# Optimization experiments

Measured on AMD Instinct MI355X. Metric: run time of the kernel, lower is better.

## Reference

```python
import jax, jax.numpy as jnp
import numpy as np

HEADS = 4
DIM_HEAD = 64
INNER = HEADS * DIM_HEAD  # 256
MAP_SIZE = (8, 8, 8)
DN = ('NCDHW', 'OIDHW', 'NCDHW')


def _depthwise3d(x, w):
    # x: [B,C,D,H,W], w: [C,1,3,3,3] (torch groups=C layout)
    return jax.lax.conv_general_dilated(
        x, w, window_strides=(1, 1, 1), padding='SAME',
        dimension_numbers=DN, feature_group_count=x.shape[1])


def _dws_conv(x, dw, pw):
    # depthwise 3x3x3 then pointwise 1x1x1 (pw: [out,in])
    y = _depthwise3d(x, dw)
    return jnp.einsum('bcdhw,oc->bodhw', y, pw)


def _split_heads(t):
    # 'b (dim_head heads) d h w -> b heads (d h w) dim_head'
    B, C, D, H, W = t.shape
    t = t.reshape(B, DIM_HEAD, HEADS, D * H * W)
    return t.transpose(0, 2, 3, 1)


def _merge_heads(t, D, H, W):
    # 'b heads n dim_head -> b (dim_head heads) d h w'
    B = t.shape[0]
    return t.transpose(0, 3, 1, 2).reshape(B, DIM_HEAD * HEADS, D, H, W)


def setup_inputs() -> dict:
    key = jax.random.key(0)
    ks = jax.random.split(key, 8)
    B, feat_dim, map_dim, out_dim = 2, 128, 64, 128
    D = H = W = 24
    s = 0.02
    return {
        'feat': jax.random.normal(ks[0], (B, feat_dim, D, H, W), jnp.float32),
        'smap': jax.random.normal(ks[1], (B, map_dim) + MAP_SIZE, jnp.float32),
        'feat_qv_dw': jax.random.normal(ks[2], (feat_dim, 1, 3, 3, 3), jnp.float32) * s,
        'feat_qv_pw': jax.random.normal(ks[3], (2 * INNER, feat_dim), jnp.float32) * s,
        'feat_out_dw': jax.random.normal(ks[4], (INNER, 1, 3, 3, 3), jnp.float32) * s,
        'feat_out_pw': jax.random.normal(ks[5], (out_dim, INNER), jnp.float32) * s,
        'map_qv_w': jax.random.normal(ks[6], (2 * INNER, map_dim), jnp.float32) * s,
        'map_out_w': jax.random.normal(ks[7], (map_dim, INNER), jnp.float32) * s,
    }


def reference(feat, smap, feat_qv_dw, feat_qv_pw, feat_out_dw, feat_out_pw,
              map_qv_w, map_out_w):
    B, C, D, H, W = feat.shape
    scale = DIM_HEAD ** -0.5

    # projections
    fqv = _dws_conv(feat, feat_qv_dw, feat_qv_pw)           # [B, 2*inner, D,H,W]
    feat_q, feat_v = jnp.split(fqv, 2, axis=1)
    mqv = jnp.einsum('bcdhw,oc->bodhw', smap, map_qv_w)     # [B, 2*inner, 8,8,8]
    map_q, map_v = jnp.split(mqv, 2, axis=1)

    feat_q, feat_v = _split_heads(feat_q), _split_heads(feat_v)  # [B,h,N,dh]
    map_q, map_v = _split_heads(map_q), _split_heads(map_v)      # [B,h,M,dh]

    # shared scores, dual-direction softmax
    attn = jnp.einsum('bhid,bhjd->bhij', feat_q, map_q) * scale  # [B,h,N,M]
    feat_map_attn = jax.nn.softmax(attn, axis=-1)
    map_feat_attn = jax.nn.softmax(attn, axis=-2)

    feat_out = jnp.einsum('bhij,bhjd->bhid', feat_map_attn, map_v)   # [B,h,N,dh]
    map_out = jnp.einsum('bhji,bhjd->bhid', map_feat_attn, feat_v)   # [B,h,M,dh]

    feat_out = _merge_heads(feat_out, D, H, W)
    map_out = _merge_heads(map_out, *MAP_SIZE)

    feat_out = _dws_conv(feat_out, feat_out_dw, feat_out_pw)   # [B,out_dim,D,H,W]
    map_out = jnp.einsum('bcdhw,oc->bodhw', map_out, map_out_w)  # [B,map_dim,8,8,8]
    return feat_out, map_out
```

## Files before the change

### kernel.cpp

```cpp
#include <hip/hip_runtime.h>

#define BB 2
#define CH_FEAT 128
#define HEADS 4
#define DH 64
#define INNER 256
#define NPOS 13824
#define MPOS 512
#define DSZ 24
#define JSPLIT 27
#define JCHUNK (NPOS / JSPLIT)

typedef __attribute__((ext_vector_type(8))) short bf16x8;
typedef __attribute__((ext_vector_type(4))) float f32x4;

__device__ inline unsigned short bf16_rn(float x) {
  unsigned u = __builtin_bit_cast(unsigned, x);
  u += 0x7FFF + ((u >> 16) & 1);
  return (unsigned short)(u >> 16);
}
__device__ inline unsigned pk_bf16(float a, float b) {
  return (unsigned)bf16_rn(a) | ((unsigned)bf16_rn(b) << 16);
}
__device__ inline float bf2f(unsigned short u) {
  return __builtin_bit_cast(float, (unsigned)u << 16);
}
__device__ inline float4 ld_bf4(const unsigned short* p) {
  uint2 u = *(const uint2*)p;
  float4 f;
  f.x = __builtin_bit_cast(float, (u.x & 0xFFFFu) << 16);
  f.y = __builtin_bit_cast(float, u.x & 0xFFFF0000u);
  f.z = __builtin_bit_cast(float, (u.y & 0xFFFFu) << 16);
  f.w = __builtin_bit_cast(float, u.y & 0xFFFF0000u);
  return f;
}

#define GL2LDS(g, l)                                                        \
  __builtin_amdgcn_global_load_lds(                                         \
      (const __attribute__((address_space(1))) void*)(g),                   \
      (__attribute__((address_space(3))) void*)(l), 16, 0, 0)

__device__ inline bf16x8 lds_frag(const char* tile, int row, int colb) {
  return *(const bf16x8*)(tile + row * 128 + (colb ^ ((row & 7) << 4)));
}
__device__ inline bf16x8 lds_fragP(const char* tile, int row, int colb, int pitch) {
  return *(const bf16x8*)(tile + row * pitch + (colb ^ ((row & 7) << 4)));
}

__global__ __launch_bounds__(512) void k_map_qv(const float* __restrict__ smap,
                                                const float* __restrict__ w,
                                                unsigned short* __restrict__ mapqb,
                                                unsigned short* __restrict__ mapvTb) {
  int bm = blockIdx.x;
  int b = bm >> 9, m = bm & 511;
  __shared__ float s[64];
  int t = threadIdx.x;
  if (t < 64) s[t] = smap[(size_t)(b * 64 + t) * MPOS + m];
  __syncthreads();
  const float* wr = w + t * 64;
  float acc = 0.f;
#pragma unroll
  for (int c = 0; c < 64; ++c) acc += wr[c] * s[c];
  int qv = t >> 8, c2 = t & 255, head = c2 & 3, dh = c2 >> 2;
  int bh = b * HEADS + head;
  if (qv == 0)
    mapqb[((size_t)bh * MPOS + m) * 64 + dh] = bf16_rn(acc * 0.125f);
  else
    mapvTb[((size_t)bh * 64 + dh) * MPOS + m] = bf16_rn(acc);
}

__global__ __launch_bounds__(256) void k_dwf(const float* __restrict__ in,
                                             const float* __restrict__ w,
                                             unsigned short* __restrict__ out, int C) {
  int tid = blockIdx.x * 256 + threadIdx.x;
  int bc = tid / 1728;
  int s = tid - bc * 1728;
  int c = bc & (C - 1);
  int xs = (s % 3) * 8;
  int row = s / 3;
  int y = row % 24, z = row / 24;
  const float* wr = w + c * 27;
  const float* ip = in + (size_t)bc * NPOS;

  float acc[8];
#pragma unroll
  for (int i = 0; i < 8; ++i) acc[i] = 0.f;

#pragma unroll
  for (int dz = 0; dz < 3; ++dz) {
#pragma unroll
    for (int dy = 0; dy < 3; ++dy) {
      int zz = z + dz - 1, yy = y + dy - 1;
      bool ok = ((unsigned)zz < 24u) && ((unsigned)yy < 24u);
      float w0 = ok ? wr[dz * 9 + dy * 3 + 0] : 0.f;
      float w1 = ok ? wr[dz * 9 + dy * 3 + 1] : 0.f;
      float w2 = ok ? wr[dz * 9 + dy * 3 + 2] : 0.f;
      int zc = min(max(zz, 0), 23), yc = min(max(yy, 0), 23);
      int ro = (zc * 24 + yc) * 24;
      float4 Bv = *(const float4*)(ip + ro + xs);
      float4 Cv = *(const float4*)(ip + ro + xs + 4);
      float xm1 = xs ? *(ip + ro + xs - 1) : 0.f;
      float x8 = (xs < 16) ? *(ip + ro + xs + 8) : 0.f;
      float xv[10] = {xm1, Bv.x, Bv.y, Bv.z, Bv.w, Cv.x, Cv.y, Cv.z, Cv.w, x8};
#pragma unroll
      for (int i = 0; i < 8; ++i)
        acc[i] += w0 * xv[i] + w1 * xv[i + 1] + w2 * xv[i + 2];
    }
  }
  unsigned short* op = out + (size_t)bc * NPOS + row * 24 + xs;
  uint4 pv;
  pv.x = pk_bf16(acc[0], acc[1]);
  pv.y = pk_bf16(acc[2], acc[3]);
  pv.z = pk_bf16(acc[4], acc[5]);
  pv.w = pk_bf16(acc[6], acc[7]);
  *(uint4*)op = pv;
}

__global__ __launch_bounds__(256) void k_dwb(const unsigned short* __restrict__ in,
                                             const float* __restrict__ w,
                                             unsigned short* __restrict__ out, int C) {
  int tid = blockIdx.x * 256 + threadIdx.x;
  int bc = tid / 1728;
  int s = tid - bc * 1728;
  int c = bc & (C - 1), b = bc / C;
  int cm = (c & 63) * 4 + (c >> 6);
  int xs = (s % 3) * 8;
  int row = s / 3;
  int y = row % 24, z = row / 24;
  const float* wr = w + cm * 27;
  const unsigned short* ip = in + (size_t)bc * NPOS;

  float acc[8];
#pragma unroll
  for (int i = 0; i < 8; ++i) acc[i] = 0.f;

#pragma unroll
  for (int dz = 0; dz < 3; ++dz) {
#pragma unroll
    for (int dy = 0; dy < 3; ++dy) {
      int zz = z + dz - 1, yy = y + dy - 1;
      bool ok = ((unsigned)zz < 24u) && ((unsigned)yy < 24u);
      float w0 = ok ? wr[dz * 9 + dy * 3 + 0] : 0.f;
      float w1 = ok ? wr[dz * 9 + dy * 3 + 1] : 0.f;
      float w2 = ok ? wr[dz * 9 + dy * 3 + 2] : 0.f;
      int zc = min(max(zz, 0), 23), yc = min(max(yy, 0), 23);
      int ro = (zc * 24 + yc) * 24;
      float4 Bv = ld_bf4(ip + ro + xs);
      float4 Cv = ld_bf4(ip + ro + xs + 4);
      float xm1 = xs ? bf2f(ip[ro + xs - 1]) : 0.f;
      float x8 = (xs < 16) ? bf2f(ip[ro + xs + 8]) : 0.f;
      float xv[10] = {xm1, Bv.x, Bv.y, Bv.z, Bv.w, Cv.x, Cv.y, Cv.z, Cv.w, x8};
#pragma unroll
      for (int i = 0; i < 8; ++i)
        acc[i] += w0 * xv[i] + w1 * xv[i + 1] + w2 * xv[i + 2];
    }
  }
  unsigned short* op = out + ((size_t)b * C + cm) * NPOS + row * 24 + xs;
  uint4 pv;
  pv.x = pk_bf16(acc[0], acc[1]);
  pv.y = pk_bf16(acc[2], acc[3]);
  pv.z = pk_bf16(acc[4], acc[5]);
  pv.w = pk_bf16(acc[6], acc[7]);
  *(uint4*)op = pv;
}

__global__ __launch_bounds__(256) void k_pwqv_m(const unsigned short* __restrict__ dwt,
                                                const float* __restrict__ pw,
                                                unsigned short* __restrict__ fqb,
                                                unsigned short* __restrict__ fvTb) {
  __shared__ __align__(16) char sW[16384];
  __shared__ __align__(16) char sR[32768];
  __shared__ __align__(16) char sB[32768];
  int t = threadIdx.x, wave = t >> 6, lane = t & 63, g = lane >> 4, c = lane & 15;
  int n0 = blockIdx.x * 128, ti = blockIdx.y, b = blockIdx.z;
  int qv = ti >> 2, head = ti & 3, bh = b * 4 + head;

  {
    int r = t >> 2, ks = (t & 3) * 32;
    int co = qv * 256 + r * 4 + head;
    const float* wp = pw + (size_t)co * 128 + ks;
    unsigned pkv[16];
#pragma unroll
    for (int i = 0; i < 8; ++i) {
      float4 v = *(const float4*)(wp + i * 4);
      pkv[2 * i] = pk_bf16(v.x, v.y);
      pkv[2 * i + 1] = pk_bf16(v.z, v.w);
    }
#pragma unroll
    for (int u = 0; u < 4; ++u) {
      int colb = (ks * 2 + u * 16) ^ ((r & 7) << 4);
      *(uint4*)(sW + r * 256 + colb) = *(uint4*)&pkv[u * 4];
    }
  }
  const char* Bgc = (const char*)(dwt + (size_t)b * CH_FEAT * NPOS);
#pragma unroll
  for (int p = 0; p < 8; ++p) {
    int oo = p * 4096 + t * 16;
    int k = oo >> 8, col = oo & 255;
    GL2LDS(Bgc + (size_t)k * (NPOS * 2) + n0 * 2 + col, sR + oo);
  }
  __syncthreads();

  {
    const unsigned short* R16 = (const unsigned short*)sR;
#pragma unroll
    for (int it = 0; it < 8; ++it) {
      int cid = it * 256 + t;
      int n = cid & 127, kc16 = (cid >> 7) & 15;
      unsigned short v[8];
#pragma unroll
      for (int j = 0; j < 8; ++j) v[j] = R16[(kc16 * 8 + j) * 128 + n];
      unsigned u4[4];
#pragma unroll
      for (int i = 0; i < 4; ++i)
        u4[i] = (unsigned)v[2 * i] | ((unsigned)v[2 * i + 1] << 16);
      *(uint4*)(sB + n * 256 + ((kc16 * 16) ^ ((n & 7) << 4))) = *(uint4*)&u4[0];
    }
  }
  __syncthreads();

  f32x4 acc[4][2];
#pragma unroll
  for (int ct = 0; ct < 4; ++ct)
#pragma unroll
    for (int jf = 0; jf < 2; ++jf) acc[ct][jf] = (f32x4){0.f, 0.f, 0.f, 0.f};
  int nw = wave * 32;
#pragma unroll
  for (int kc = 0; kc < 4; ++kc) {
    bf16x8 bq[2];
#pragma unroll
    for (int jf = 0; jf < 2; ++jf)
      bq[jf] = lds_fragP(sB, nw + jf * 16 + c, kc * 64 + g * 16, 256);
#pragma unroll
    for (int ct = 0; ct < 4; ++ct) {
      bf16x8 a = lds_fragP(sW, ct * 16 + c, kc * 64 + g * 16, 256);
#pragma unroll
      for (int jf = 0; jf < 2; ++jf)
        acc[ct][jf] = __builtin_amdgcn_mfma_f32_16x16x32_bf16(a, bq[jf], acc[ct][jf], 0, 0, 0);
    }
  }
  __syncthreads();

  char* dmp = sR;
#pragma unroll
  for (int ct = 0; ct < 4; ++ct)
#pragma unroll
    for (int jf = 0; jf < 2; ++jf) {
      int n = nw + jf * 16 + c;
      uint2 wv;
      wv.x = pk_bf16(acc[ct][jf][0], acc[ct][jf][1]);
      wv.y = pk_bf16(acc[ct][jf][2], acc[ct][jf][3]);
      *(uint2*)(dmp + n * 144 + (ct * 16 + 4 * g) * 2) = wv;
    }
  __syncthreads();

  if (qv == 0) {
    int nr = t >> 1, seg = t & 1;
    const char* src = dmp + nr * 144 + seg * 64;
    unsigned short* dst = fqb + ((size_t)bh * NPOS + n0 + nr) * 64 + seg * 32;
#pragma unroll
    for (int i = 0; i < 4; ++i)
      *(uint4*)(dst + i * 8) = *(const uint4*)(src + i * 16);
  } else {
#pragma unroll
    for (int it = 0; it < 2; ++it) {
      int idx = it * 256 + t;
      int dh = idx >> 3, nseg = (idx & 7) * 16;
      unsigned pkv[8];
#pragma unroll
      for (int i = 0; i < 8; ++i) {
        unsigned short lo = *(const unsigned short*)(dmp + (nseg + 2 * i) * 144 + dh * 2);
        unsigned short hi = *(const unsigned short*)(dmp + (nseg + 2 * i + 1) * 144 + dh * 2);
        pkv[i] = (unsigned)lo | ((unsigned)hi << 16);
      }
      unsigned short* dst = fvTb + ((size_t)bh * 64 + dh) * NPOS + n0 + nseg;
      *(uint4*)(dst) = *(uint4*)&pkv[0];
      *(uint4*)(dst + 8) = *(uint4*)&pkv[4];
    }
  }
}

__global__ __launch_bounds__(256) void k_pwout_m(const unsigned short* __restrict__ dwo,
                                                 const float* __restrict__ pw,
                                                 float* __restrict__ out1) {
  __shared__ __align__(16) char sW[32768];
  __shared__ __align__(16) char sB[32768];
  __shared__ __align__(16) char sR[16384];
  int t = threadIdx.x, wave = t >> 6, lane = t & 63, g = lane >> 4, c = lane & 15;
  int n0 = blockIdx.x * 128, ti = blockIdx.y, b = blockIdx.z;

  {
    int r = t >> 2, ks = (t & 3) * 64;
    const float* wp = pw + (size_t)(ti * 64 + r) * 256 + ks;
    unsigned pkv[32];
#pragma unroll
    for (int i = 0; i < 16; ++i) {
      float4 v = *(const float4*)(wp + i * 4);
      pkv[2 * i] = pk_bf16(v.x, v.y);
      pkv[2 * i + 1] = pk_bf16(v.z, v.w);
    }
#pragma unroll
    for (int u = 0; u < 8; ++u) {
      int colb = (ks * 2 + u * 16) ^ ((r & 7) << 4);
      *(uint4*)(sW + r * 512 + colb) = *(uint4*)&pkv[u * 4];
    }
  }

  f32x4 acc[4][2];
#pragma unroll
  for (int ct = 0; ct < 4; ++ct)
#pragma unroll
    for (int jf = 0; jf < 2; ++jf) acc[ct][jf] = (f32x4){0.f, 0.f, 0.f, 0.f};
  int nw = wave * 32;
  const char* Bgc = (const char*)(dwo + (size_t)b * INNER * NPOS);
  const unsigned short* R16 = (const unsigned short*)sR;

  for (int kh = 0; kh < 2; ++kh) {
#pragma unroll
    for (int q = 0; q < 2; ++q) {
#pragma unroll
      for (int p = 0; p < 4; ++p) {
        int oo = p * 4096 + t * 16;
        int kl = oo >> 8, col = oo & 255;
        GL2LDS(Bgc + (size_t)(kh * 128 + q * 64 + kl) * (NPOS * 2) + n0 * 2 + col,
               sR + oo);
      }
      __syncthreads();
#pragma unroll
      for (int it = 0; it < 4; ++it) {
        int cid = it * 256 + t;
        int n = cid & 127, kcl = (cid >> 7) & 7;
        unsigned short v[8];
#pragma unroll
        for (int j = 0; j < 8; ++j) v[j] = R16[(kcl * 8 + j) * 128 + n];
        unsigned u4[4];
#pragma unroll
        for (int i = 0; i < 4; ++i)
          u4[i] = (unsigned)v[2 * i] | ((unsigned)v[2 * i + 1] << 16);
        int kc16 = q * 8 + kcl;
        *(uint4*)(sB + n * 256 + ((kc16 * 16) ^ ((n & 7) << 4))) = *(uint4*)&u4[0];
      }
      __syncthreads();
    }
#pragma unroll
    for (int kc = 0; kc < 4; ++kc) {
      bf16x8 bq[2];
#pragma unroll
      for (int jf = 0; jf < 2; ++jf)
        bq[jf] = lds_fragP(sB, nw + jf * 16 + c, kc * 64 + g * 16, 256);
#pragma unroll
      for (int ct = 0; ct < 4; ++ct) {
        bf16x8 a = lds_fragP(sW, ct * 16 + c, (kh * 4 + kc) * 64 + g * 16, 512);
#pragma unroll
        for (int jf = 0; jf < 2; ++jf)
          acc[ct][jf] = __builtin_amdgcn_mfma_f32_16x16x32_bf16(a, bq[jf], acc[ct][jf], 0, 0, 0);
      }
    }
    __syncthreads();
  }
#pragma unroll
  for (int ct = 0; ct < 4; ++ct)
#pragma unroll
    for (int jf = 0; jf < 2; ++jf) {
      int n = n0 + nw + jf * 16 + c;
#pragma unroll
      for (int r = 0; r < 4; ++r) {
        int co = ti * 64 + ct * 16 + 4 * g + r;
        out1[((size_t)b * 128 + co) * NPOS + n] = acc[ct][jf][r];
      }
    }
}

__global__ __launch_bounds__(256) void k_attn_row(const unsigned short* __restrict__ fqb,
                                                  const unsigned short* __restrict__ mapqb,
                                                  const unsigned short* __restrict__ mapvTb,
                                                  unsigned short* __restrict__ F) {
  __shared__ __align__(16) char sPool[32768];
  __shared__ __align__(16) unsigned sP[4][2][16][36];
  __shared__ float sL[4][2][16];
  int t = threadIdx.x, wave = t >> 6, lane = t & 63, g = lane >> 4, c = lane & 15;
  int bh = blockIdx.y;
  int j0 = blockIdx.x * 128 + wave * 32;

  const char* Kg = (const char*)(mapqb + (size_t)bh * MPOS * 64);
  const char* Vg = (const char*)(mapvTb + (size_t)bh * 64 * MPOS);

  const unsigned short* fqp = fqb + ((size_t)bh * NPOS + j0 + c) * 64 + 8 * g;
  bf16x8 bq00 = *(const bf16x8*)(fqp);
  bf16x8 bq01 = *(const bf16x8*)(fqp + 32);
  bf16x8 bq10 = *(const bf16x8*)(fqp + 16 * 64);
  bf16x8 bq11 = *(const bf16x8*)(fqp + 16 * 64 + 32);

  f32x4 o[2][4];
#pragma unroll
  for (int jf = 0; jf < 2; ++jf)
#pragma unroll
    for (int dt = 0; dt < 4; ++dt) o[jf][dt] = (f32x4){0.f, 0.f, 0.f, 0.f};
  float ls0 = 0.f, ls1 = 0.f;

#pragma unroll
  for (int p = 0; p < 2; ++p) {
    int oo = p * 4096 + t * 16;
    int row = oo >> 7, col = (oo & 127) ^ (((oo >> 7) & 7) << 4);
    GL2LDS(Kg + (size_t)row * 128 + col, sPool + oo);
    GL2LDS(Vg + (size_t)row * 1024 + col, sPool + 16384 + oo);
  }
  __syncthreads();

  for (int ic = 0; ic < 8; ++ic) {
    const char* Kt = sPool + (ic & 1) * 8192;
    const char* Vt = sPool + 16384 + (ic & 1) * 8192;
    if (ic < 7) {
      int ibase = (ic + 1) * 64;
      int bsel = ((ic + 1) & 1) * 8192;
#pragma unroll
      for (int p = 0; p < 2; ++p) {
        int oo = p * 4096 + t * 16;
        int row = oo >> 7, col = (oo & 127) ^ (((oo >> 7) & 7) << 4);
        GL2LDS(Kg + (size_t)(ibase + row) * 128 + col, sPool + bsel + oo);
        GL2LDS(Vg + (size_t)row * 1024 + ibase * 2 + col, sPool + 16384 + bsel + oo);
      }
    }
#pragma unroll
    for (int ti = 0; ti < 4; ++ti) {
      bf16x8 a0 = lds_frag(Kt, ti * 16 + c, 16 * g);
      bf16x8 a1 = lds_frag(Kt, ti * 16 + c, 64 + 16 * g);
      f32x4 s0 = {0.f, 0.f, 0.f, 0.f}, s1 = {0.f, 0.f, 0.f, 0.f};
      s0 = __builtin_amdgcn_mfma_f32_16x16x32_bf16(a0, bq00, s0, 0, 0, 0);
      s0 = __builtin_amdgcn_mfma_f32_16x16x32_bf16(a1, bq01, s0, 0, 0, 0);
      s1 = __builtin_amdgcn_mfma_f32_16x16x32_bf16(a0, bq10, s1, 0, 0, 0);
      s1 = __builtin_amdgcn_mfma_f32_16x16x32_bf16(a1, bq11, s1, 0, 0, 0);
      float p0 = __expf(s0[0]), p1 = __expf(s0[1]), p2 = __expf(s0[2]), p3 = __expf(s0[3]);
      ls0 += (p0 + p1) + (p2 + p3);
      sP[wave][0][c][ti * 8 + 2 * g] = pk_bf16(p0, p1);
      sP[wave][0][c][ti * 8 + 2 * g + 1] = pk_bf16(p2, p3);
      float q0 = __expf(s1[0]), q1 = __expf(s1[1]), q2 = __expf(s1[2]), q3 = __expf(s1[3]);
      ls1 += (q0 + q1) + (q2 + q3);
      sP[wave][1][c][ti * 8 + 2 * g] = pk_bf16(q0, q1);
      sP[wave][1][c][ti * 8 + 2 * g + 1] = pk_bf16(q2, q3);
    }
#pragma unroll
    for (int ks = 0; ks < 2; ++ks) {
      bf16x8 ap0 = *(const bf16x8*)&sP[wave][0][c][ks * 16 + 4 * g];
      bf16x8 ap1 = *(const bf16x8*)&sP[wave][1][c][ks * 16 + 4 * g];
#pragma unroll
      for (int dt = 0; dt < 4; ++dt) {
        bf16x8 bv = lds_frag(Vt, dt * 16 + c, ks * 64 + 16 * g);
        o[0][dt] = __builtin_amdgcn_mfma_f32_16x16x32_bf16(ap0, bv, o[0][dt], 0, 0, 0);
        o[1][dt] = __builtin_amdgcn_mfma_f32_16x16x32_bf16(ap1, bv, o[1][dt], 0, 0, 0);
      }
    }
    __syncthreads();
  }

  ls0 += __shfl_xor(ls0, 16); ls0 += __shfl_xor(ls0, 32);
  ls1 += __shfl_xor(ls1, 16); ls1 += __shfl_xor(ls1, 32);
  if (g == 0) { sL[wave][0][c] = 1.f / ls0; sL[wave][1][c] = 1.f / ls1; }
#pragma unroll
  for (int jf = 0; jf < 2; ++jf) {
    float rl0 = sL[wave][jf][4 * g + 0], rl1 = sL[wave][jf][4 * g + 1];
    float rl2 = sL[wave][jf][4 * g + 2], rl3 = sL[wave][jf][4 * g + 3];
#pragma unroll
    for (int dt = 0; dt < 4; ++dt) {
      uint2 wv;
      wv.x = pk_bf16(o[jf][dt][0] * rl0, o[jf][dt][1] * rl1);
      wv.y = pk_bf16(o[jf][dt][2] * rl2, o[jf][dt][3] * rl3);
      *(uint2*)(sPool + (dt * 16 + c) * 272 + (wave * 32 + jf * 16 + 4 * g) * 2) = wv;
    }
  }
  __syncthreads();
  {
    int ch = t >> 2, seg = t & 3;
    int b = bh >> 2, head = bh & 3;
    unsigned short* dst = F + ((size_t)b * INNER + head * 64 + ch) * NPOS +
                          blockIdx.x * 128 + seg * 32;
    const char* src = sPool + ch * 272 + seg * 64;
#pragma unroll
    for (int i = 0; i < 4; ++i)
      *(uint4*)(dst + i * 8) = *(const uint4*)(src + i * 16);
  }
}

__global__ __launch_bounds__(256) void k_attn_col(const unsigned short* __restrict__ fqb,
                                                  const unsigned short* __restrict__ fvTb,
                                                  const unsigned short* __restrict__ mapqb,
                                                  float* __restrict__ Gc,
                                                  float* __restrict__ Gl) {
  __shared__ __align__(16) char sQ[2][8192];
  __shared__ __align__(16) char sV[2][8192];
  __shared__ __align__(16) unsigned sP[4][2][16][36];
  int t = threadIdx.x, wave = t >> 6, lane = t & 63, g = lane >> 4, c = lane & 15;
  int bh = blockIdx.x, chunk = blockIdx.z;
  int i0 = blockIdx.y * 128 + wave * 32;
  int jb = chunk * JCHUNK;

  const char* Qg = (const char*)(fqb + (size_t)bh * NPOS * 64);
  const char* Vg = (const char*)(fvTb + (size_t)bh * 64 * NPOS);

  const unsigned short* kp = mapqb + ((size_t)bh * MPOS + i0 + c) * 64 + 8 * g;
  bf16x8 bm00 = *(const bf16x8*)(kp);
  bf16x8 bm01 = *(const bf16x8*)(kp + 32);
  bf16x8 bm10 = *(const bf16x8*)(kp + 16 * 64);
  bf16x8 bm11 = *(const bf16x8*)(kp + 16 * 64 + 32);

  f32x4 o[2][4];
#pragma unroll
  for (int f = 0; f < 2; ++f)
#pragma unroll
    for (int dt = 0; dt < 4; ++dt) o[f][dt] = (f32x4){0.f, 0.f, 0.f, 0.f};
  float lc0 = 0.f, lc1 = 0.f;

#pragma unroll
  for (int p = 0; p < 2; ++p) {
    int oo = p * 4096 + t * 16;
    int row = oo >> 7, col = (oo & 127) ^ (((oo >> 7) & 7) << 4);
    GL2LDS(Qg + (size_t)(jb + row) * 128 + col, sQ[0] + oo);
    GL2LDS(Vg + (size_t)row * (NPOS * 2) + jb * 2 + col, sV[0] + oo);
  }
  __syncthreads();

  for (int jc = 0; jc < JCHUNK / 64; ++jc) {
    const char* Qt = sQ[jc & 1];
    const char* Vt = sV[jc & 1];
    if (jc < JCHUNK / 64 - 1) {
      int jbase = jb + (jc + 1) * 64;
#pragma unroll
      for (int p = 0; p < 2; ++p) {
        int oo = p * 4096 + t * 16;
        int row = oo >> 7, col = (oo & 127) ^ (((oo >> 7) & 7) << 4);
        GL2LDS(Qg + (size_t)(jbase + row) * 128 + col, sQ[(jc + 1) & 1] + oo);
        GL2LDS(Vg + (size_t)row * (NPOS * 2) + jbase * 2 + col, sV[(jc + 1) & 1] + oo);
      }
    }
#pragma unroll
    for (int tj = 0; tj < 4; ++tj) {
      bf16x8 a0 = lds_frag(Qt, tj * 16 + c, 16 * g);
      bf16x8 a1 = lds_frag(Qt, tj * 16 + c, 64 + 16 * g);
      f32x4 s0 = {0.f, 0.f, 0.f, 0.f}, s1 = {0.f, 0.f, 0.f, 0.f};
      s0 = __builtin_amdgcn_mfma_f32_16x16x32_bf16(a0, bm00, s0, 0, 0, 0);
      s0 = __builtin_amdgcn_mfma_f32_16x16x32_bf16(a1, bm01, s0, 0, 0, 0);
      s1 = __builtin_amdgcn_mfma_f32_16x16x32_bf16(a0, bm10, s1, 0, 0, 0);
      s1 = __builtin_amdgcn_mfma_f32_16x16x32_bf16(a1, bm11, s1, 0, 0, 0);
      float p0 = __expf(s0[0]), p1 = __expf(s0[1]), p2 = __expf(s0[2]), p3 = __expf(s0[3]);
      lc0 += (p0 + p1) + (p2 + p3);
      sP[wave][0][c][tj * 8 + 2 * g] = pk_bf16(p0, p1);
      sP[wave][0][c][tj * 8 + 2 * g + 1] = pk_bf16(p2, p3);
      float q0 = __expf(s1[0]), q1 = __expf(s1[1]), q2 = __expf(s1[2]), q3 = __expf(s1[3]);
      lc1 += (q0 + q1) + (q2 + q3);
      sP[wave][1][c][tj * 8 + 2 * g] = pk_bf16(q0, q1);
      sP[wave][1][c][tj * 8 + 2 * g + 1] = pk_bf16(q2, q3);
    }
#pragma unroll
    for (int ks = 0; ks < 2; ++ks) {
      bf16x8 ap0 = *(const bf16x8*)&sP[wave][0][c][ks * 16 + 4 * g];
      bf16x8 ap1 = *(const bf16x8*)&sP[wave][1][c][ks * 16 + 4 * g];
#pragma unroll
      for (int dt = 0; dt < 4; ++dt) {
        bf16x8 bv = lds_frag(Vt, dt * 16 + c, ks * 64 + 16 * g);
        o[0][dt] = __builtin_amdgcn_mfma_f32_16x16x32_bf16(ap0, bv, o[0][dt], 0, 0, 0);
        o[1][dt] = __builtin_amdgcn_mfma_f32_16x16x32_bf16(ap1, bv, o[1][dt], 0, 0, 0);
      }
    }
    __syncthreads();
  }

  lc0 += __shfl_xor(lc0, 16); lc0 += __shfl_xor(lc0, 32);
  lc1 += __shfl_xor(lc1, 16); lc1 += __shfl_xor(lc1, 32);
  int gi = chunk * 8 + bh;
  if (g == 0) {
    Gl[(size_t)gi * MPOS + i0 + c] = lc0;
    Gl[(size_t)gi * MPOS + i0 + 16 + c] = lc1;
  }
  float* gp = Gc + ((size_t)gi * MPOS + i0) * 64;
#pragma unroll
  for (int f = 0; f < 2; ++f)
#pragma unroll
    for (int dt = 0; dt < 4; ++dt)
#pragma unroll
      for (int r = 0; r < 4; ++r)
        gp[(size_t)(f * 16 + 4 * g + r) * 64 + dt * 16 + c] = o[f][dt][r];
}

__global__ __launch_bounds__(256) void k_map_out(const float* __restrict__ Gc,
                                                 const float* __restrict__ Gl,
                                                 const float* __restrict__ mow,
                                                 float* __restrict__ out2) {
  int m = blockIdx.x, b = blockIdx.y, t = threadIdx.x;
  __shared__ float sMA[256];
  __shared__ float sL[4];
  if (t < 4) {
    float l = 0.f;
#pragma unroll 4
    for (int ch = 0; ch < JSPLIT; ++ch) l += Gl[(size_t)(ch * 8 + b * 4 + t) * MPOS + m];
    sL[t] = 1.f / l;
  }
  __syncthreads();
  {
    int head = t & 3, dh = t >> 2;
    int bh = b * 4 + head;
    float a = 0.f;
#pragma unroll 4
    for (int ch = 0; ch < JSPLIT; ++ch)
      a += Gc[((size_t)(ch * 8 + bh) * MPOS + m) * 64 + dh];
    sMA[t] = a * sL[head];
  }
  __syncthreads();
  if (t < 64) {
    const float* wr = mow + t * 256;
    float acc = 0.f;
#pragma unroll 4
    for (int c = 0; c < 256; ++c) acc += wr[c] * sMA[c];
    out2[((size_t)b * 64 + t) * MPOS + m] = acc;
  }
}

extern "C" void kernel_launch(void* const* d_in, const int* in_sizes, int n_in,
                              void* d_out, int out_size, void* d_ws, size_t ws_size,
                              hipStream_t stream) {
  const float* feat = (const float*)d_in[0];
  const float* smap = (const float*)d_in[1];
  const float* fqv_dw = (const float*)d_in[2];
  const float* fqv_pw = (const float*)d_in[3];
  const float* fout_dw = (const float*)d_in[4];
  const float* fout_pw = (const float*)d_in[5];
  const float* mqv_w = (const float*)d_in[6];
  const float* mout_w = (const float*)d_in[7];

  float* out = (float*)d_out;
  float* out1 = out;
  float* out2 = out + (size_t)BB * 128 * NPOS;

  const size_t QV = (size_t)BB * HEADS * NPOS * DH;
  const size_t MQV = (size_t)BB * HEADS * MPOS * DH;
  float* ws = (float*)d_ws;
  unsigned short* F = (unsigned short*)ws;
  unsigned short* fqb = (unsigned short*)(ws + QV);
  unsigned short* fvTb = fqb + QV;
  unsigned short* mapqb = fvTb + QV;
  unsigned short* mapvTb = mapqb + MQV;
  float* Gc = (float*)(mapvTb + MQV);
  float* Gl = Gc + (size_t)JSPLIT * 8 * MPOS * 64;

  unsigned short* dwt = (unsigned short*)out1;
  unsigned short* dwt2 = fqb;

  k_map_qv<<<dim3(BB * MPOS), dim3(512), 0, stream>>>(smap, mqv_w, mapqb, mapvTb);
  k_dwf<<<dim3(BB * CH_FEAT * 1728 / 256), dim3(256), 0, stream>>>(feat, fqv_dw, dwt, CH_FEAT);
  k_pwqv_m<<<dim3(NPOS / 128, 8, BB), dim3(256), 0, stream>>>(dwt, fqv_pw, fqb, fvTb);
  k_attn_row<<<dim3(NPOS / 128, BB * HEADS), dim3(256), 0, stream>>>(fqb, mapqb, mapvTb, F);
  k_attn_col<<<dim3(8, MPOS / 128, JSPLIT), dim3(256), 0, stream>>>(fqb, fvTb, mapqb, Gc, Gl);
  k_map_out<<<dim3(MPOS, BB), dim3(256), 0, stream>>>(Gc, Gl, mout_w, out2);
  k_dwb<<<dim3(BB * INNER * 1728 / 256), dim3(256), 0, stream>>>(F, fout_dw, dwt2, INNER);
  k_pwout_m<<<dim3(NPOS / 128, 2, BB), dim3(256), 0, stream>>>(dwt2, fout_pw, out1);
}
```

Before: 195.9 us.

## Merge independent kernels into combined launches via block-index dispatch

Three kernel pairs that don't depend on each other now each share one launch, with the block index choosing the branch: map QV projection with the first depthwise conv, row and column attention, and map output projection with the second depthwise conv. This cuts the launch count from eight to five, removes the gaps between back-to-back launches, and lets the small grids run alongside the large ones. The merged kernels take the larger shared-memory footprint and register pressure of either branch, which can lower occupancy for the lighter branch.

```diff
diff --git a/kernel.cpp b/kernel.cpp
--- a/kernel.cpp
+++ b/kernel.cpp
@@ -47,121 +47,77 @@
   return *(const bf16x8*)(tile + row * pitch + (colb ^ ((row & 7) << 4)));
 }
 
-__global__ __launch_bounds__(512) void k_map_qv(const float* __restrict__ smap,
-                                                const float* __restrict__ w,
-                                                unsigned short* __restrict__ mapqb,
-                                                unsigned short* __restrict__ mapvTb) {
-  int bm = blockIdx.x;
-  int b = bm >> 9, m = bm & 511;
-  __shared__ float s[64];
+__global__ __launch_bounds__(256) void k_pre(const float* __restrict__ smap,
+                                             const float* __restrict__ mqv_w,
+                                             unsigned short* __restrict__ mapqb,
+                                             unsigned short* __restrict__ mapvTb,
+                                             const float* __restrict__ feat,
+                                             const float* __restrict__ fqv_dw,
+                                             unsigned short* __restrict__ dwt) {
+  int bid = blockIdx.x;
   int t = threadIdx.x;
-  if (t < 64) s[t] = smap[(size_t)(b * 64 + t) * MPOS + m];
-  __syncthreads();
-  const float* wr = w + t * 64;
-  float acc = 0.f;
-#pragma unroll
-  for (int c = 0; c < 64; ++c) acc += wr[c] * s[c];
-  int qv = t >> 8, c2 = t & 255, head = c2 & 3, dh = c2 >> 2;
-  int bh = b * HEADS + head;
-  if (qv == 0)
-    mapqb[((size_t)bh * MPOS + m) * 64 + dh] = bf16_rn(acc * 0.125f);
-  else
-    mapvTb[((size_t)bh * 64 + dh) * MPOS + m] = bf16_rn(acc);
-}
-
-__global__ __launch_bounds__(256) void k_dwf(const float* __restrict__ in,
-                                             const float* __restrict__ w,
-                                             unsigned short* __restrict__ out, int C) {
-  int tid = blockIdx.x * 256 + threadIdx.x;
-  int bc = tid / 1728;
-  int s = tid - bc * 1728;
-  int c = bc & (C - 1);
-  int xs = (s % 3) * 8;
-  int row = s / 3;
-  int y = row % 24, z = row / 24;
-  const float* wr = w + c * 27;
-  const float* ip = in + (size_t)bc * NPOS;
-
-  float acc[8];
-#pragma unroll
-  for (int i = 0; i < 8; ++i) acc[i] = 0.f;
-
-#pragma unroll
-  for (int dz = 0; dz < 3; ++dz) {
-#pragma unroll
-    for (int dy = 0; dy < 3; ++dy) {
-      int zz = z + dz - 1, yy = y + dy - 1;
-      bool ok = ((unsigned)zz < 24u) && ((unsigned)yy < 24u);
-      float w0 = ok ? wr[dz * 9 + dy * 3 + 0] : 0.f;
-      float w1 = ok ? wr[dz * 9 + dy * 3 + 1] : 0.f;
-      float w2 = ok ? wr[dz * 9 + dy * 3 + 2] : 0.f;
-      int zc = min(max(zz, 0), 23), yc = min(max(yy, 0), 23);
-      int ro = (zc * 24 + yc) * 24;
-      float4 Bv = *(const float4*)(ip + ro + xs);
-      float4 Cv = *(const float4*)(ip + ro + xs + 4);
-      float xm1 = xs ? *(ip + ro + xs - 1) : 0.f;
-      float x8 = (xs < 16) ? *(ip + ro + xs + 8) : 0.f;
-      float xv[10] = {xm1, Bv.x, Bv.y, Bv.z, Bv.w, Cv.x, Cv.y, Cv.z, Cv.w, x8};
-#pragma unroll
-      for (int i = 0; i < 8; ++i)
-        acc[i] += w0 * xv[i] + w1 * xv[i + 1] + w2 * xv[i + 2];
-    }
-  }
-  unsigned short* op = out + (size_t)bc * NPOS + row * 24 + xs;
-  uint4 pv;
-  pv.x = pk_bf16(acc[0], acc[1]);
-  pv.y = pk_bf16(acc[2], acc[3]);
-  pv.z = pk_bf16(acc[4], acc[5]);
-  pv.w = pk_bf16(acc[6], acc[7]);
-  *(uint4*)op = pv;
-}
-
-__global__ __launch_bounds__(256) void k_dwb(const unsigned short* __restrict__ in,
-                                             const float* __restrict__ w,
-                                             unsigned short* __restrict__ out, int C) {
-  int tid = blockIdx.x * 256 + threadIdx.x;
-  int bc = tid / 1728;
-  int s = tid - bc * 1728;
-  int c = bc & (C - 1), b = bc / C;
-  int cm = (c & 63) * 4 + (c >> 6);
-  int xs = (s % 3) * 8;
-  int row = s / 3;
-  int y = row % 24, z = row / 24;
-  const float* wr = w + cm * 27;
-  const unsigned short* ip = in + (size_t)bc * NPOS;
-
-  float acc[8];
-#pragma unroll
-  for (int i = 0; i < 8; ++i) acc[i] = 0.f;
-
-#pragma unroll
-  for (int dz = 0; dz < 3; ++dz) {
-#pragma unroll
-    for (int dy = 0; dy < 3; ++dy) {
-      int zz = z + dz - 1, yy = y + dy - 1;
-      bool ok = ((unsigned)zz < 24u) && ((unsigned)yy < 24u);
-      float w0 = ok ? wr[dz * 9 + dy * 3 + 0] : 0.f;
-      float w1 = ok ? wr[dz * 9 + dy * 3 + 1] : 0.f;
-      float w2 = ok ? wr[dz * 9 + dy * 3 + 2] : 0.f;
-      int zc = min(max(zz, 0), 23), yc = min(max(yy, 0), 23);
-      int ro = (zc * 24 + yc) * 24;
-      float4 Bv = ld_bf4(ip + ro + xs);
-      float4 Cv = ld_bf4(ip + ro + xs + 4);
-      float xm1 = xs ? bf2f(ip[ro + xs - 1]) : 0.f;
-      float x8 = (xs < 16) ? bf2f(ip[ro + xs + 8]) : 0.f;
-      float xv[10] = {xm1, Bv.x, Bv.y, Bv.z, Bv.w, Cv.x, Cv.y, Cv.z, Cv.w, x8};
-#pragma unroll
-      for (int i = 0; i < 8; ++i)
-        acc[i] += w0 * xv[i] + w1 * xv[i + 1] + w2 * xv[i + 2];
-    }
-  }
-  unsigned short* op = out + ((size_t)b * C + cm) * NPOS + row * 24 + xs;
-  uint4 pv;
-  pv.x = pk_bf16(acc[0], acc[1]);
-  pv.y = pk_bf16(acc[2], acc[3]);
-  pv.z = pk_bf16(acc[4], acc[5]);
-  pv.w = pk_bf16(acc[6], acc[7]);
-  *(uint4*)op = pv;
+  if (bid < 1024) {
+    int b = bid >> 9, m = bid & 511;
+    __shared__ float s[64];
+    if (t < 64) s[t] = smap[(size_t)(b * 64 + t) * MPOS + m];
+    __syncthreads();
+#pragma unroll
+    for (int half = 0; half < 2; ++half) {
+      int co2 = half * 256 + t;
+      const float* wr = mqv_w + (size_t)co2 * 64;
+      float acc = 0.f;
+#pragma unroll
+      for (int c = 0; c < 64; ++c) acc += wr[c] * s[c];
+      int qv = co2 >> 8, c2 = co2 & 255, head = c2 & 3, dh = c2 >> 2;
+      int bh = b * HEADS + head;
+      if (qv == 0)
+        mapqb[((size_t)bh * MPOS + m) * 64 + dh] = bf16_rn(acc * 0.125f);
+      else
+        mapvTb[((size_t)bh * 64 + dh) * MPOS + m] = bf16_rn(acc);
+    }
+  } else {
+    int tid = (bid - 1024) * 256 + t;
+    int bc = tid / 1728;
+    int s = tid - bc * 1728;
+    int c = bc & (CH_FEAT - 1);
+    int xs = (s % 3) * 8;
+    int row = s / 3;
+    int y = row % 24, z = row / 24;
+    const float* wr = fqv_dw + c * 27;
+    const float* ip = feat + (size_t)bc * NPOS;
+
+    float acc[8];
+#pragma unroll
+    for (int i = 0; i < 8; ++i) acc[i] = 0.f;
+#pragma unroll
+    for (int dz = 0; dz < 3; ++dz) {
+#pragma unroll
+      for (int dy = 0; dy < 3; ++dy) {
+        int zz = z + dz - 1, yy = y + dy - 1;
+        bool ok = ((unsigned)zz < 24u) && ((unsigned)yy < 24u);
+        float w0 = ok ? wr[dz * 9 + dy * 3 + 0] : 0.f;
+        float w1 = ok ? wr[dz * 9 + dy * 3 + 1] : 0.f;
+        float w2 = ok ? wr[dz * 9 + dy * 3 + 2] : 0.f;
+        int zc = min(max(zz, 0), 23), yc = min(max(yy, 0), 23);
+        int ro = (zc * 24 + yc) * 24;
+        float4 Bv = *(const float4*)(ip + ro + xs);
+        float4 Cv = *(const float4*)(ip + ro + xs + 4);
+        float xm1 = xs ? *(ip + ro + xs - 1) : 0.f;
+        float x8 = (xs < 16) ? *(ip + ro + xs + 8) : 0.f;
+        float xv[10] = {xm1, Bv.x, Bv.y, Bv.z, Bv.w, Cv.x, Cv.y, Cv.z, Cv.w, x8};
+#pragma unroll
+        for (int i = 0; i < 8; ++i)
+          acc[i] += w0 * xv[i] + w1 * xv[i + 1] + w2 * xv[i + 2];
+      }
+    }
+    unsigned short* op = dwt + (size_t)bc * NPOS + row * 24 + xs;
+    uint4 pv;
+    pv.x = pk_bf16(acc[0], acc[1]);
+    pv.y = pk_bf16(acc[2], acc[3]);
+    pv.z = pk_bf16(acc[4], acc[5]);
+    pv.w = pk_bf16(acc[6], acc[7]);
+    *(uint4*)op = pv;
+  }
 }
 
 __global__ __launch_bounds__(256) void k_pwqv_m(const unsigned short* __restrict__ dwt,
@@ -280,6 +236,302 @@
   }
 }
 
+__global__ __launch_bounds__(256) void k_attn(const unsigned short* __restrict__ fqb,
+                                              const unsigned short* __restrict__ fvTb,
+                                              const unsigned short* __restrict__ mapqb,
+                                              const unsigned short* __restrict__ mapvTb,
+                                              unsigned short* __restrict__ F,
+                                              float* __restrict__ Gc,
+                                              float* __restrict__ Gl) {
+  __shared__ __align__(16) char sPool[32768];
+  __shared__ __align__(16) unsigned sP[4][2][16][36];
+  __shared__ __align__(16) float sL[4][2][16];
+  int bid = blockIdx.x;
+  int t = threadIdx.x, wave = t >> 6, lane = t & 63, g = lane >> 4, c = lane & 15;
+
+  if (bid < 864) {
+    int jblk = bid % 108, bh = bid / 108;
+    int j0 = jblk * 128 + wave * 32;
+
+    const char* Kg = (const char*)(mapqb + (size_t)bh * MPOS * 64);
+    const char* Vg = (const char*)(mapvTb + (size_t)bh * 64 * MPOS);
+
+    const unsigned short* fqp = fqb + ((size_t)bh * NPOS + j0 + c) * 64 + 8 * g;
+    bf16x8 bq00 = *(const bf16x8*)(fqp);
+    bf16x8 bq01 = *(const bf16x8*)(fqp + 32);
+    bf16x8 bq10 = *(const bf16x8*)(fqp + 16 * 64);
+    bf16x8 bq11 = *(const bf16x8*)(fqp + 16 * 64 + 32);
+
+    f32x4 o[2][4];
+#pragma unroll
+    for (int jf = 0; jf < 2; ++jf)
+#pragma unroll
+      for (int dt = 0; dt < 4; ++dt) o[jf][dt] = (f32x4){0.f, 0.f, 0.f, 0.f};
+    float ls0 = 0.f, ls1 = 0.f;
+
+#pragma unroll
+    for (int p = 0; p < 2; ++p) {
+      int oo = p * 4096 + t * 16;
+      int row = oo >> 7, col = (oo & 127) ^ (((oo >> 7) & 7) << 4);
+      GL2LDS(Kg + (size_t)row * 128 + col, sPool + oo);
+      GL2LDS(Vg + (size_t)row * 1024 + col, sPool + 16384 + oo);
+    }
+    __syncthreads();
+
+    for (int ic = 0; ic < 8; ++ic) {
+      const char* Kt = sPool + (ic & 1) * 8192;
+      const char* Vt = sPool + 16384 + (ic & 1) * 8192;
+      if (ic < 7) {
+        int ibase = (ic + 1) * 64;
+        int bsel = ((ic + 1) & 1) * 8192;
+#pragma unroll
+        for (int p = 0; p < 2; ++p) {
+          int oo = p * 4096 + t * 16;
+          int row = oo >> 7, col = (oo & 127) ^ (((oo >> 7) & 7) << 4);
+          GL2LDS(Kg + (size_t)(ibase + row) * 128 + col, sPool + bsel + oo);
+          GL2LDS(Vg + (size_t)row * 1024 + ibase * 2 + col, sPool + 16384 + bsel + oo);
+        }
+      }
+#pragma unroll
+      for (int ti = 0; ti < 4; ++ti) {
+        bf16x8 a0 = lds_frag(Kt, ti * 16 + c, 16 * g);
+        bf16x8 a1 = lds_frag(Kt, ti * 16 + c, 64 + 16 * g);
+        f32x4 s0 = {0.f, 0.f, 0.f, 0.f}, s1 = {0.f, 0.f, 0.f, 0.f};
+        s0 = __builtin_amdgcn_mfma_f32_16x16x32_bf16(a0, bq00, s0, 0, 0, 0);
+        s0 = __builtin_amdgcn_mfma_f32_16x16x32_bf16(a1, bq01, s0, 0, 0, 0);
+        s1 = __builtin_amdgcn_mfma_f32_16x16x32_bf16(a0, bq10, s1, 0, 0, 0);
+        s1 = __builtin_amdgcn_mfma_f32_16x16x32_bf16(a1, bq11, s1, 0, 0, 0);
+        float p0 = __expf(s0[0]), p1 = __expf(s0[1]), p2 = __expf(s0[2]), p3 = __expf(s0[3]);
+        ls0 += (p0 + p1) + (p2 + p3);
+        sP[wave][0][c][ti * 8 + 2 * g] = pk_bf16(p0, p1);
+        sP[wave][0][c][ti * 8 + 2 * g + 1] = pk_bf16(p2, p3);
+        float q0 = __expf(s1[0]), q1 = __expf(s1[1]), q2 = __expf(s1[2]), q3 = __expf(s1[3]);
+        ls1 += (q0 + q1) + (q2 + q3);
+        sP[wave][1][c][ti * 8 + 2 * g] = pk_bf16(q0, q1);
+        sP[wave][1][c][ti * 8 + 2 * g + 1] = pk_bf16(q2, q3);
+      }
+#pragma unroll
+      for (int ks = 0; ks < 2; ++ks) {
+        bf16x8 ap0 = *(const bf16x8*)&sP[wave][0][c][ks * 16 + 4 * g];
+        bf16x8 ap1 = *(const bf16x8*)&sP[wave][1][c][ks * 16 + 4 * g];
+#pragma unroll
+        for (int dt = 0; dt < 4; ++dt) {
+          bf16x8 bv = lds_frag(Vt, dt * 16 + c, ks * 64 + 16 * g);
+          o[0][dt] = __builtin_amdgcn_mfma_f32_16x16x32_bf16(ap0, bv, o[0][dt], 0, 0, 0);
+          o[1][dt] = __builtin_amdgcn_mfma_f32_16x16x32_bf16(ap1, bv, o[1][dt], 0, 0, 0);
+        }
+      }
+      __syncthreads();
+    }
+
+    ls0 += __shfl_xor(ls0, 16); ls0 += __shfl_xor(ls0, 32);
+    ls1 += __shfl_xor(ls1, 16); ls1 += __shfl_xor(ls1, 32);
+    if (g == 0) { sL[wave][0][c] = 1.f / ls0; sL[wave][1][c] = 1.f / ls1; }
+#pragma unroll
+    for (int jf = 0; jf < 2; ++jf) {
+      float rl0 = sL[wave][jf][4 * g + 0], rl1 = sL[wave][jf][4 * g + 1];
+      float rl2 = sL[wave][jf][4 * g + 2], rl3 = sL[wave][jf][4 * g + 3];
+#pragma unroll
+      for (int dt = 0; dt < 4; ++dt) {
+        uint2 wv;
+        wv.x = pk_bf16(o[jf][dt][0] * rl0, o[jf][dt][1] * rl1);
+        wv.y = pk_bf16(o[jf][dt][2] * rl2, o[jf][dt][3] * rl3);
+        *(uint2*)(sPool + (dt * 16 + c) * 272 + (wave * 32 + jf * 16 + 4 * g) * 2) = wv;
+      }
+    }
+    __syncthreads();
+    {
+      int ch = t >> 2, seg = t & 3;
+      int b = bh >> 2, head = bh & 3;
+      unsigned short* dst = F + ((size_t)b * INNER + head * 64 + ch) * NPOS +
+                            jblk * 128 + seg * 32;
+      const char* src = sPool + ch * 272 + seg * 64;
+#pragma unroll
+      for (int i = 0; i < 4; ++i)
+        *(uint4*)(dst + i * 8) = *(const uint4*)(src + i * 16);
+    }
+  } else {
+    int cid = bid - 864;
+    int bh = cid & 7, iblk = (cid >> 3) & 3, chunk = cid >> 5;
+    char* sQ = sPool;
+    char* sV = sPool + 16384;
+    int i0 = iblk * 128 + wave * 32;
+    int jb = chunk * JCHUNK;
+
+    const char* Qg = (const char*)(fqb + (size_t)bh * NPOS * 64);
+    const char* Vg = (const char*)(fvTb + (size_t)bh * 64 * NPOS);
+
+    const unsigned short* kp = mapqb + ((size_t)bh * MPOS + i0 + c) * 64 + 8 * g;
+    bf16x8 bm00 = *(const bf16x8*)(kp);
+    bf16x8 bm01 = *(const bf16x8*)(kp + 32);
+    bf16x8 bm10 = *(const bf16x8*)(kp + 16 * 64);
+    bf16x8 bm11 = *(const bf16x8*)(kp + 16 * 64 + 32);
+
+    f32x4 o[2][4];
+#pragma unroll
+    for (int f = 0; f < 2; ++f)
+#pragma unroll
+      for (int dt = 0; dt < 4; ++dt) o[f][dt] = (f32x4){0.f, 0.f, 0.f, 0.f};
+    float lc0 = 0.f, lc1 = 0.f;
+
+#pragma unroll
+    for (int p = 0; p < 2; ++p) {
+      int oo = p * 4096 + t * 16;
+      int row = oo >> 7, col = (oo & 127) ^ (((oo >> 7) & 7) << 4);
+      GL2LDS(Qg + (size_t)(jb + row) * 128 + col, sQ + oo);
+      GL2LDS(Vg + (size_t)row * (NPOS * 2) + jb * 2 + col, sV + oo);
+    }
+    __syncthreads();
+
+    for (int jc = 0; jc < JCHUNK / 64; ++jc) {
+      const char* Qt = sQ + (jc & 1) * 8192;
+      const char* Vt = sV + (jc & 1) * 8192;
+      if (jc < JCHUNK / 64 - 1) {
+        int jbase = jb + (jc + 1) * 64;
+        int bsel = ((jc + 1) & 1) * 8192;
+#pragma unroll
+        for (int p = 0; p < 2; ++p) {
+          int oo = p * 4096 + t * 16;
+          int row = oo >> 7, col = (oo & 127) ^ (((oo >> 7) & 7) << 4);
+          GL2LDS(Qg + (size_t)(jbase + row) * 128 + col, sQ + bsel + oo);
+          GL2LDS(Vg + (size_t)row * (NPOS * 2) + jbase * 2 + col, sV + bsel + oo);
+        }
+      }
+#pragma unroll
+      for (int tj = 0; tj < 4; ++tj) {
+        bf16x8 a0 = lds_frag(Qt, tj * 16 + c, 16 * g);
+        bf16x8 a1 = lds_frag(Qt, tj * 16 + c, 64 + 16 * g);
+        f32x4 s0 = {0.f, 0.f, 0.f, 0.f}, s1 = {0.f, 0.f, 0.f, 0.f};
+        s0 = __builtin_amdgcn_mfma_f32_16x16x32_bf16(a0, bm00, s0, 0, 0, 0);
+        s0 = __builtin_amdgcn_mfma_f32_16x16x32_bf16(a1, bm01, s0, 0, 0, 0);
+        s1 = __builtin_amdgcn_mfma_f32_16x16x32_bf16(a0, bm10, s1, 0, 0, 0);
+        s1 = __builtin_amdgcn_mfma_f32_16x16x32_bf16(a1, bm11, s1, 0, 0, 0);
+        float p0 = __expf(s0[0]), p1 = __expf(s0[1]), p2 = __expf(s0[2]), p3 = __expf(s0[3]);
+        lc0 += (p0 + p1) + (p2 + p3);
+        sP[wave][0][c][tj * 8 + 2 * g] = pk_bf16(p0, p1);
+        sP[wave][0][c][tj * 8 + 2 * g + 1] = pk_bf16(p2, p3);
+        float q0 = __expf(s1[0]), q1 = __expf(s1[1]), q2 = __expf(s1[2]), q3 = __expf(s1[3]);
+        lc1 += (q0 + q1) + (q2 + q3);
+        sP[wave][1][c][tj * 8 + 2 * g] = pk_bf16(q0, q1);
+        sP[wave][1][c][tj * 8 + 2 * g + 1] = pk_bf16(q2, q3);
+      }
+#pragma unroll
+      for (int ks = 0; ks < 2; ++ks) {
+        bf16x8 ap0 = *(const bf16x8*)&sP[wave][0][c][ks * 16 + 4 * g];
+        bf16x8 ap1 = *(const bf16x8*)&sP[wave][1][c][ks * 16 + 4 * g];
+#pragma unroll
+        for (int dt = 0; dt < 4; ++dt) {
+          bf16x8 bv = lds_frag(Vt, dt * 16 + c, ks * 64 + 16 * g);
+          o[0][dt] = __builtin_amdgcn_mfma_f32_16x16x32_bf16(ap0, bv, o[0][dt], 0, 0, 0);
+          o[1][dt] = __builtin_amdgcn_mfma_f32_16x16x32_bf16(ap1, bv, o[1][dt], 0, 0, 0);
+        }
+      }
+      __syncthreads();
+    }
+
+    lc0 += __shfl_xor(lc0, 16); lc0 += __shfl_xor(lc0, 32);
+    lc1 += __shfl_xor(lc1, 16); lc1 += __shfl_xor(lc1, 32);
+    int gi = chunk * 8 + bh;
+    if (g == 0) {
+      Gl[(size_t)gi * MPOS + i0 + c] = lc0;
+      Gl[(size_t)gi * MPOS + i0 + 16 + c] = lc1;
+    }
+    float* gp = Gc + ((size_t)gi * MPOS + i0) * 64;
+#pragma unroll
+    for (int f = 0; f < 2; ++f)
+#pragma unroll
+      for (int dt = 0; dt < 4; ++dt)
+#pragma unroll
+        for (int r = 0; r < 4; ++r)
+          gp[(size_t)(f * 16 + 4 * g + r) * 64 + dt * 16 + c] = o[f][dt][r];
+  }
+}
+
+__global__ __launch_bounds__(256) void k_post(const unsigned short* __restrict__ F,
+                                              const float* __restrict__ fout_dw,
+                                              unsigned short* __restrict__ dwt2,
+                                              const float* __restrict__ Gc,
+                                              const float* __restrict__ Gl,
+                                              const float* __restrict__ mow,
+                                              float* __restrict__ out2) {
+  int bid = blockIdx.x;
+  int t = threadIdx.x;
+  if (bid < 3456) {
+    int tid = bid * 256 + t;
+    int bc = tid / 1728;
+    int s = tid - bc * 1728;
+    int c = bc & (INNER - 1), b = bc / INNER;
+    int cm = (c & 63) * 4 + (c >> 6);
+    int xs = (s % 3) * 8;
+    int row = s / 3;
+    int y = row % 24, z = row / 24;
+    const float* wr = fout_dw + cm * 27;
+    const unsigned short* ip = F + (size_t)bc * NPOS;
+
+    float acc[8];
+#pragma unroll
+    for (int i = 0; i < 8; ++i) acc[i] = 0.f;
+#pragma unroll
+    for (int dz = 0; dz < 3; ++dz) {
+#pragma unroll
+      for (int dy = 0; dy < 3; ++dy) {
+        int zz = z + dz - 1, yy = y + dy - 1;
+        bool ok = ((unsigned)zz < 24u) && ((unsigned)yy < 24u);
+        float w0 = ok ? wr[dz * 9 + dy * 3 + 0] : 0.f;
+        float w1 = ok ? wr[dz * 9 + dy * 3 + 1] : 0.f;
+        float w2 = ok ? wr[dz * 9 + dy * 3 + 2] : 0.f;
+        int zc = min(max(zz, 0), 23), yc = min(max(yy, 0), 23);
+        int ro = (zc * 24 + yc) * 24;
+        float4 Bv = ld_bf4(ip + ro + xs);
+        float4 Cv = ld_bf4(ip + ro + xs + 4);
+        float xm1 = xs ? bf2f(ip[ro + xs - 1]) : 0.f;
+        float x8 = (xs < 16) ? bf2f(ip[ro + xs + 8]) : 0.f;
+        float xv[10] = {xm1, Bv.x, Bv.y, Bv.z, Bv.w, Cv.x, Cv.y, Cv.z, Cv.w, x8};
+#pragma unroll
+        for (int i = 0; i < 8; ++i)
+          acc[i] += w0 * xv[i] + w1 * xv[i + 1] + w2 * xv[i + 2];
+      }
+    }
+    unsigned short* op = dwt2 + ((size_t)b * INNER + cm) * NPOS + row * 24 + xs;
+    uint4 pv;
+    pv.x = pk_bf16(acc[0], acc[1]);
+    pv.y = pk_bf16(acc[2], acc[3]);
+    pv.z = pk_bf16(acc[4], acc[5]);
+    pv.w = pk_bf16(acc[6], acc[7]);
+    *(uint4*)op = pv;
+  } else {
+    int mi = bid - 3456;
+    int m = mi & 511, b = mi >> 9;
+    __shared__ float sMA[256];
+    __shared__ float sL2[4];
+    if (t < 4) {
+      float l = 0.f;
+#pragma unroll 4
+      for (int ch = 0; ch < JSPLIT; ++ch)
+        l += Gl[(size_t)(ch * 8 + b * 4 + t) * MPOS + m];
+      sL2[t] = 1.f / l;
+    }
+    __syncthreads();
+    {
+      int head = t & 3, dh = t >> 2;
+      int bh = b * 4 + head;
+      float a = 0.f;
+#pragma unroll 4
+      for (int ch = 0; ch < JSPLIT; ++ch)
+        a += Gc[((size_t)(ch * 8 + bh) * MPOS + m) * 64 + dh];
+      sMA[t] = a * sL2[head];
+    }
+    __syncthreads();
+    if (t < 64) {
+      const float* wr = mow + t * 256;
+      float acc = 0.f;
+#pragma unroll 4
+      for (int c = 0; c < 256; ++c) acc += wr[c] * sMA[c];
+      out2[((size_t)b * 64 + t) * MPOS + m] = acc;
+    }
+  }
+}
+
 __global__ __launch_bounds__(256) void k_pwout_m(const unsigned short* __restrict__ dwo,
                                                  const float* __restrict__ pw,
                                                  float* __restrict__ out1) {
@@ -369,249 +621,6 @@
         out1[((size_t)b * 128 + co) * NPOS + n] = acc[ct][jf][r];
       }
     }
-}
-
-__global__ __launch_bounds__(256) void k_attn_row(const unsigned short* __restrict__ fqb,
-                                                  const unsigned short* __restrict__ mapqb,
-                                                  const unsigned short* __restrict__ mapvTb,
-                                                  unsigned short* __restrict__ F) {
-  __shared__ __align__(16) char sPool[32768];
-  __shared__ __align__(16) unsigned sP[4][2][16][36];
-  __shared__ float sL[4][2][16];
-  int t = threadIdx.x, wave = t >> 6, lane = t & 63, g = lane >> 4, c = lane & 15;
-  int bh = blockIdx.y;
-  int j0 = blockIdx.x * 128 + wave * 32;
-
-  const char* Kg = (const char*)(mapqb + (size_t)bh * MPOS * 64);
-  const char* Vg = (const char*)(mapvTb + (size_t)bh * 64 * MPOS);
-
-  const unsigned short* fqp = fqb + ((size_t)bh * NPOS + j0 + c) * 64 + 8 * g;
-  bf16x8 bq00 = *(const bf16x8*)(fqp);
-  bf16x8 bq01 = *(const bf16x8*)(fqp + 32);
-  bf16x8 bq10 = *(const bf16x8*)(fqp + 16 * 64);
-  bf16x8 bq11 = *(const bf16x8*)(fqp + 16 * 64 + 32);
-
-  f32x4 o[2][4];
-#pragma unroll
-  for (int jf = 0; jf < 2; ++jf)
-#pragma unroll
-    for (int dt = 0; dt < 4; ++dt) o[jf][dt] = (f32x4){0.f, 0.f, 0.f, 0.f};
-  float ls0 = 0.f, ls1 = 0.f;
-
-#pragma unroll
-  for (int p = 0; p < 2; ++p) {
-    int oo = p * 4096 + t * 16;
-    int row = oo >> 7, col = (oo & 127) ^ (((oo >> 7) & 7) << 4);
-    GL2LDS(Kg + (size_t)row * 128 + col, sPool + oo);
-    GL2LDS(Vg + (size_t)row * 1024 + col, sPool + 16384 + oo);
-  }
-  __syncthreads();
-
-  for (int ic = 0; ic < 8; ++ic) {
-    const char* Kt = sPool + (ic & 1) * 8192;
-    const char* Vt = sPool + 16384 + (ic & 1) * 8192;
-    if (ic < 7) {
-      int ibase = (ic + 1) * 64;
-      int bsel = ((ic + 1) & 1) * 8192;
-#pragma unroll
-      for (int p = 0; p < 2; ++p) {
-        int oo = p * 4096 + t * 16;
-        int row = oo >> 7, col = (oo & 127) ^ (((oo >> 7) & 7) << 4);
-        GL2LDS(Kg + (size_t)(ibase + row) * 128 + col, sPool + bsel + oo);
-        GL2LDS(Vg + (size_t)row * 1024 + ibase * 2 + col, sPool + 16384 + bsel + oo);
-      }
-    }
-#pragma unroll
-    for (int ti = 0; ti < 4; ++ti) {
-      bf16x8 a0 = lds_frag(Kt, ti * 16 + c, 16 * g);
-      bf16x8 a1 = lds_frag(Kt, ti * 16 + c, 64 + 16 * g);
-      f32x4 s0 = {0.f, 0.f, 0.f, 0.f}, s1 = {0.f, 0.f, 0.f, 0.f};
-      s0 = __builtin_amdgcn_mfma_f32_16x16x32_bf16(a0, bq00, s0, 0, 0, 0);
-      s0 = __builtin_amdgcn_mfma_f32_16x16x32_bf16(a1, bq01, s0, 0, 0, 0);
-      s1 = __builtin_amdgcn_mfma_f32_16x16x32_bf16(a0, bq10, s1, 0, 0, 0);
-      s1 = __builtin_amdgcn_mfma_f32_16x16x32_bf16(a1, bq11, s1, 0, 0, 0);
-      float p0 = __expf(s0[0]), p1 = __expf(s0[1]), p2 = __expf(s0[2]), p3 = __expf(s0[3]);
-      ls0 += (p0 + p1) + (p2 + p3);
-      sP[wave][0][c][ti * 8 + 2 * g] = pk_bf16(p0, p1);
-      sP[wave][0][c][ti * 8 + 2 * g + 1] = pk_bf16(p2, p3);
-      float q0 = __expf(s1[0]), q1 = __expf(s1[1]), q2 = __expf(s1[2]), q3 = __expf(s1[3]);
-      ls1 += (q0 + q1) + (q2 + q3);
-      sP[wave][1][c][ti * 8 + 2 * g] = pk_bf16(q0, q1);
-      sP[wave][1][c][ti * 8 + 2 * g + 1] = pk_bf16(q2, q3);
-    }
-#pragma unroll
-    for (int ks = 0; ks < 2; ++ks) {
-      bf16x8 ap0 = *(const bf16x8*)&sP[wave][0][c][ks * 16 + 4 * g];
-      bf16x8 ap1 = *(const bf16x8*)&sP[wave][1][c][ks * 16 + 4 * g];
-#pragma unroll
-      for (int dt = 0; dt < 4; ++dt) {
-        bf16x8 bv = lds_frag(Vt, dt * 16 + c, ks * 64 + 16 * g);
-        o[0][dt] = __builtin_amdgcn_mfma_f32_16x16x32_bf16(ap0, bv, o[0][dt], 0, 0, 0);
-        o[1][dt] = __builtin_amdgcn_mfma_f32_16x16x32_bf16(ap1, bv, o[1][dt], 0, 0, 0);
-      }
-    }
-    __syncthreads();
-  }
-
-  ls0 += __shfl_xor(ls0, 16); ls0 += __shfl_xor(ls0, 32);
-  ls1 += __shfl_xor(ls1, 16); ls1 += __shfl_xor(ls1, 32);
-  if (g == 0) { sL[wave][0][c] = 1.f / ls0; sL[wave][1][c] = 1.f / ls1; }
-#pragma unroll
-  for (int jf = 0; jf < 2; ++jf) {
-    float rl0 = sL[wave][jf][4 * g + 0], rl1 = sL[wave][jf][4 * g + 1];
-    float rl2 = sL[wave][jf][4 * g + 2], rl3 = sL[wave][jf][4 * g + 3];
-#pragma unroll
-    for (int dt = 0; dt < 4; ++dt) {
-      uint2 wv;
-      wv.x = pk_bf16(o[jf][dt][0] * rl0, o[jf][dt][1] * rl1);
-      wv.y = pk_bf16(o[jf][dt][2] * rl2, o[jf][dt][3] * rl3);
-      *(uint2*)(sPool + (dt * 16 + c) * 272 + (wave * 32 + jf * 16 + 4 * g) * 2) = wv;
-    }
-  }
-  __syncthreads();
-  {
-    int ch = t >> 2, seg = t & 3;
-    int b = bh >> 2, head = bh & 3;
-    unsigned short* dst = F + ((size_t)b * INNER + head * 64 + ch) * NPOS +
-                          blockIdx.x * 128 + seg * 32;
-    const char* src = sPool + ch * 272 + seg * 64;
-#pragma unroll
-    for (int i = 0; i < 4; ++i)
-      *(uint4*)(dst + i * 8) = *(const uint4*)(src + i * 16);
-  }
-}
-
-__global__ __launch_bounds__(256) void k_attn_col(const unsigned short* __restrict__ fqb,
-                                                  const unsigned short* __restrict__ fvTb,
-                                                  const unsigned short* __restrict__ mapqb,
-                                                  float* __restrict__ Gc,
-                                                  float* __restrict__ Gl) {
-  __shared__ __align__(16) char sQ[2][8192];
-  __shared__ __align__(16) char sV[2][8192];
-  __shared__ __align__(16) unsigned sP[4][2][16][36];
-  int t = threadIdx.x, wave = t >> 6, lane = t & 63, g = lane >> 4, c = lane & 15;
-  int bh = blockIdx.x, chunk = blockIdx.z;
-  int i0 = blockIdx.y * 128 + wave * 32;
-  int jb = chunk * JCHUNK;
-
-  const char* Qg = (const char*)(fqb + (size_t)bh * NPOS * 64);
-  const char* Vg = (const char*)(fvTb + (size_t)bh * 64 * NPOS);
-
-  const unsigned short* kp = mapqb + ((size_t)bh * MPOS + i0 + c) * 64 + 8 * g;
-  bf16x8 bm00 = *(const bf16x8*)(kp);
-  bf16x8 bm01 = *(const bf16x8*)(kp + 32);
-  bf16x8 bm10 = *(const bf16x8*)(kp + 16 * 64);
-  bf16x8 bm11 = *(const bf16x8*)(kp + 16 * 64 + 32);
-
-  f32x4 o[2][4];
-#pragma unroll
-  for (int f = 0; f < 2; ++f)
-#pragma unroll
-    for (int dt = 0; dt < 4; ++dt) o[f][dt] = (f32x4){0.f, 0.f, 0.f, 0.f};
-  float lc0 = 0.f, lc1 = 0.f;
-
-#pragma unroll
-  for (int p = 0; p < 2; ++p) {
-    int oo = p * 4096 + t * 16;
-    int row = oo >> 7, col = (oo & 127) ^ (((oo >> 7) & 7) << 4);
-    GL2LDS(Qg + (size_t)(jb + row) * 128 + col, sQ[0] + oo);
-    GL2LDS(Vg + (size_t)row * (NPOS * 2) + jb * 2 + col, sV[0] + oo);
-  }
-  __syncthreads();
-
-  for (int jc = 0; jc < JCHUNK / 64; ++jc) {
-    const char* Qt = sQ[jc & 1];
-    const char* Vt = sV[jc & 1];
-    if (jc < JCHUNK / 64 - 1) {
-      int jbase = jb + (jc + 1) * 64;
-#pragma unroll
-      for (int p = 0; p < 2; ++p) {
-        int oo = p * 4096 + t * 16;
-        int row = oo >> 7, col = (oo & 127) ^ (((oo >> 7) & 7) << 4);
-        GL2LDS(Qg + (size_t)(jbase + row) * 128 + col, sQ[(jc + 1) & 1] + oo);
-        GL2LDS(Vg + (size_t)row * (NPOS * 2) + jbase * 2 + col, sV[(jc + 1) & 1] + oo);
-      }
-    }
-#pragma unroll
-    for (int tj = 0; tj < 4; ++tj) {
-      bf16x8 a0 = lds_frag(Qt, tj * 16 + c, 16 * g);
-      bf16x8 a1 = lds_frag(Qt, tj * 16 + c, 64 + 16 * g);
-      f32x4 s0 = {0.f, 0.f, 0.f, 0.f}, s1 = {0.f, 0.f, 0.f, 0.f};
-      s0 = __builtin_amdgcn_mfma_f32_16x16x32_bf16(a0, bm00, s0, 0, 0, 0);
-      s0 = __builtin_amdgcn_mfma_f32_16x16x32_bf16(a1, bm01, s0, 0, 0, 0);
-      s1 = __builtin_amdgcn_mfma_f32_16x16x32_bf16(a0, bm10, s1, 0, 0, 0);
-      s1 = __builtin_amdgcn_mfma_f32_16x16x32_bf16(a1, bm11, s1, 0, 0, 0);
-      float p0 = __expf(s0[0]), p1 = __expf(s0[1]), p2 = __expf(s0[2]), p3 = __expf(s0[3]);
-      lc0 += (p0 + p1) + (p2 + p3);
-      sP[wave][0][c][tj * 8 + 2 * g] = pk_bf16(p0, p1);
-      sP[wave][0][c][tj * 8 + 2 * g + 1] = pk_bf16(p2, p3);
-      float q0 = __expf(s1[0]), q1 = __expf(s1[1]), q2 = __expf(s1[2]), q3 = __expf(s1[3]);
-      lc1 += (q0 + q1) + (q2 + q3);
-      sP[wave][1][c][tj * 8 + 2 * g] = pk_bf16(q0, q1);
-      sP[wave][1][c][tj * 8 + 2 * g + 1] = pk_bf16(q2, q3);
-    }
-#pragma unroll
-    for (int ks = 0; ks < 2; ++ks) {
-      bf16x8 ap0 = *(const bf16x8*)&sP[wave][0][c][ks * 16 + 4 * g];
-      bf16x8 ap1 = *(const bf16x8*)&sP[wave][1][c][ks * 16 + 4 * g];
-#pragma unroll
-      for (int dt = 0; dt < 4; ++dt) {
-        bf16x8 bv = lds_frag(Vt, dt * 16 + c, ks * 64 + 16 * g);
-        o[0][dt] = __builtin_amdgcn_mfma_f32_16x16x32_bf16(ap0, bv, o[0][dt], 0, 0, 0);
-        o[1][dt] = __builtin_amdgcn_mfma_f32_16x16x32_bf16(ap1, bv, o[1][dt], 0, 0, 0);
-      }
-    }
-    __syncthreads();
-  }
-
-  lc0 += __shfl_xor(lc0, 16); lc0 += __shfl_xor(lc0, 32);
-  lc1 += __shfl_xor(lc1, 16); lc1 += __shfl_xor(lc1, 32);
-  int gi = chunk * 8 + bh;
-  if (g == 0) {
-    Gl[(size_t)gi * MPOS + i0 + c] = lc0;
-    Gl[(size_t)gi * MPOS + i0 + 16 + c] = lc1;
-  }
-  float* gp = Gc + ((size_t)gi * MPOS + i0) * 64;
-#pragma unroll
-  for (int f = 0; f < 2; ++f)
-#pragma unroll
-    for (int dt = 0; dt < 4; ++dt)
-#pragma unroll
-      for (int r = 0; r < 4; ++r)
-        gp[(size_t)(f * 16 + 4 * g + r) * 64 + dt * 16 + c] = o[f][dt][r];
-}
-
-__global__ __launch_bounds__(256) void k_map_out(const float* __restrict__ Gc,
-                                                 const float* __restrict__ Gl,
-                                                 const float* __restrict__ mow,
-                                                 float* __restrict__ out2) {
-  int m = blockIdx.x, b = blockIdx.y, t = threadIdx.x;
-  __shared__ float sMA[256];
-  __shared__ float sL[4];
-  if (t < 4) {
-    float l = 0.f;
-#pragma unroll 4
-    for (int ch = 0; ch < JSPLIT; ++ch) l += Gl[(size_t)(ch * 8 + b * 4 + t) * MPOS + m];
-    sL[t] = 1.f / l;
-  }
-  __syncthreads();
-  {
-    int head = t & 3, dh = t >> 2;
-    int bh = b * 4 + head;
-    float a = 0.f;
-#pragma unroll 4
-    for (int ch = 0; ch < JSPLIT; ++ch)
-      a += Gc[((size_t)(ch * 8 + bh) * MPOS + m) * 64 + dh];
-    sMA[t] = a * sL[head];
-  }
-  __syncthreads();
-  if (t < 64) {
-    const float* wr = mow + t * 256;
-    float acc = 0.f;
-#pragma unroll 4
-    for (int c = 0; c < 256; ++c) acc += wr[c] * sMA[c];
-    out2[((size_t)b * 64 + t) * MPOS + m] = acc;
-  }
 }
 
 extern "C" void kernel_launch(void* const* d_in, const int* in_sizes, int n_in,
@@ -644,12 +653,12 @@
   unsigned short* dwt = (unsigned short*)out1;
   unsigned short* dwt2 = fqb;
 
-  k_map_qv<<<dim3(BB * MPOS), dim3(512), 0, stream>>>(smap, mqv_w, mapqb, mapvTb);
-  k_dwf<<<dim3(BB * CH_FEAT * 1728 / 256), dim3(256), 0, stream>>>(feat, fqv_dw, dwt, CH_FEAT);
+  k_pre<<<dim3(1024 + BB * CH_FEAT * 1728 / 256), dim3(256), 0, stream>>>(
+      smap, mqv_w, mapqb, mapvTb, feat, fqv_dw, dwt);
   k_pwqv_m<<<dim3(NPOS / 128, 8, BB), dim3(256), 0, stream>>>(dwt, fqv_pw, fqb, fvTb);
-  k_attn_row<<<dim3(NPOS / 128, BB * HEADS), dim3(256), 0, stream>>>(fqb, mapqb, mapvTb, F);
-  k_attn_col<<<dim3(8, MPOS / 128, JSPLIT), dim3(256), 0, stream>>>(fqb, fvTb, mapqb, Gc, Gl);
-  k_map_out<<<dim3(MPOS, BB), dim3(256), 0, stream>>>(Gc, Gl, mout_w, out2);
-  k_dwb<<<dim3(BB * INNER * 1728 / 256), dim3(256), 0, stream>>>(F, fout_dw, dwt2, INNER);
+  k_attn<<<dim3(864 + 8 * (MPOS / 128) * JSPLIT), dim3(256), 0, stream>>>(
+      fqb, fvTb, mapqb, mapvTb, F, Gc, Gl);
+  k_post<<<dim3(BB * INNER * 1728 / 256 + BB * MPOS), dim3(256), 0, stream>>>(
+      F, fout_dw, dwt2, Gc, Gl, mout_w, out2);
   k_pwout_m<<<dim3(NPOS / 128, 2, BB), dim3(256), 0, stream>>>(dwt2, fout_pw, out1);
 }
```

Result: faster. 182.5 us (-6.8%).
